# Performance work log

Measured on AMD Instinct MI355X. Metric: run time of the kernel, lower is better.

Reference implementation:

```python
import jax, jax.numpy as jnp
import numpy as np

L, H, V, T, E = 12, 12, 50257, 1024, 768
DH = E // H
EPS = 1e-5


def _ln(x, g, b):
    mu = jnp.mean(x, axis=-1, keepdims=True)
    var = jnp.mean(jnp.square(x - mu), axis=-1, keepdims=True)
    return g * (x - mu) * jax.lax.rsqrt(var + EPS) + b


def _gelu(x):
    # tanh-approx gelu as in the source
    return 0.5 * x * (1.0 + jnp.tanh(jnp.sqrt(2.0 / jnp.pi) * (x + 0.044715 * jnp.power(x, 3))))


def setup_inputs() -> dict:
    key = jax.random.key(0)
    ks = jax.random.split(key, 12)
    s = 0.02
    return {
        "x": jax.random.randint(ks[0], (8, T), 0, V),
        "tok_emb": jax.random.normal(ks[1], (V, E), jnp.float32) * s,
        "pos_emb": jax.random.normal(ks[2], (T, E), jnp.float32) * s,
        "ln1_g": jnp.ones((L, E), jnp.float32),
        "ln1_b": jnp.zeros((L, E), jnp.float32),
        "Wqkv": jax.random.normal(ks[3], (L, E, 3 * E), jnp.float32) * s,
        "bqkv": jnp.zeros((L, 3 * E), jnp.float32),
        "Wo": jax.random.normal(ks[4], (L, E, E), jnp.float32) * s,
        "bo": jnp.zeros((L, E), jnp.float32),
        "ln2_g": jnp.ones((L, E), jnp.float32),
        "ln2_b": jnp.zeros((L, E), jnp.float32),
        "W1": jax.random.normal(ks[5], (L, E, 4 * E), jnp.float32) * s,
        "b1": jnp.zeros((L, 4 * E), jnp.float32),
        "W2": jax.random.normal(ks[6], (L, 4 * E, E), jnp.float32) * s,
        "b2": jnp.zeros((L, E), jnp.float32),
        "lnf_g": jnp.ones((E,), jnp.float32),
        "lnf_b": jnp.zeros((E,), jnp.float32),
    }


def _gpt2(x, tok_emb, pos_emb, ln1_g, ln1_b, Wqkv, bqkv, Wo, bo,
          ln2_g, ln2_b, W1, b1, W2, b2, lnf_g, lnf_b):
    B, S = x.shape
    h = tok_emb[x] + pos_emb[:S][None, :, :]  # [B,S,E]
    mask = (jnp.arange(S)[:, None] >= jnp.arange(S)[None, :]).astype(jnp.float32)  # [S,S]
    mask = mask[None, None]  # [1,1,S,S]
    scale = jax.lax.rsqrt(jnp.float32(DH))
    for l in range(L):
        a = _ln(h, ln1_g[l], ln1_b[l])
        qkv = jnp.einsum('bse,ef->bsf', a, Wqkv[l]) + bqkv[l]
        q, k, v = jnp.split(qkv, 3, axis=-1)
        q = q.reshape(B, S, H, DH).transpose(0, 2, 1, 3)
        k = k.reshape(B, S, H, DH).transpose(0, 2, 1, 3)
        v = v.reshape(B, S, H, DH).transpose(0, 2, 1, 3)
        w = jnp.einsum('bhqd,bhkd->bhqk', q, k) * scale
        w = w * mask - 1e10 * (1.0 - mask)
        w = jax.nn.softmax(w, axis=-1)
        ctx = jnp.einsum('bhqk,bhkd->bhqd', w, v)
        ctx = ctx.transpose(0, 2, 1, 3).reshape(B, S, E)
        h = h + jnp.einsum('bse,ef->bsf', ctx, Wo[l]) + bo[l]
        a2 = _ln(h, ln2_g[l], ln2_b[l])
        ff = _gelu(jnp.einsum('bse,ef->bsf', a2, W1[l]) + b1[l])
        h = h + jnp.einsum('bsf,fe->bse', ff, W2[l]) + b2[l]
    h = _ln(h, lnf_g, lnf_b)
    last = h[:, -1, :]  # [B,E]
    return jnp.matmul(last, tok_emb.T)  # [B,V]


def reference(x, tok_emb, pos_emb, ln1_g, ln1_b, Wqkv, bqkv, Wo, bo,
              ln2_g, ln2_b, W1, b1, W2, b2, lnf_g, lnf_b):
    return _gpt2(x, tok_emb, pos_emb, ln1_g, ln1_b, Wqkv, bqkv, Wo, bo,
                 ln2_g, ln2_b, W1, b1, W2, b2, lnf_g, lnf_b)
```

## Files before the change

kernel.cpp:

```cpp
#include <hip/hip_runtime.h>
#include <math.h>

#define LNUM 12
#define HNUM 12
#define EMB 768
#define TSEQ 1024
#define BBATCH 8
#define VOCAB 50257
#define NTOK (BBATCH*TSEQ)

typedef unsigned short u16;
typedef __bf16 bf16_8 __attribute__((ext_vector_type(8)));
typedef float f32x4 __attribute__((ext_vector_type(4)));

__device__ __forceinline__ u16 f2bf(float f){
  unsigned u = __float_as_uint(f);
  u += 0x7fffu + ((u >> 16) & 1u);
  return (u16)(u >> 16);
}
__device__ __forceinline__ float wred(float v){
  #pragma unroll
  for (int m = 32; m; m >>= 1) v += __shfl_xor(v, m, 64);
  return v;
}

#define GLOAD_LDS16(g, l) \
  __builtin_amdgcn_global_load_lds((const __attribute__((address_space(1))) void*)(g), \
                                   (__attribute__((address_space(3))) void*)(l), 16, 0, 0)

template<int N> struct WCst { static constexpr int val = N; };

__global__ __launch_bounds__(256) void tcvt_kernel(const float* __restrict__ src,
                                                   u16* __restrict__ dst, int K, int N){
  __shared__ float tile[32][33];
  size_t off = (size_t)blockIdx.z * K * N;
  const float* s = src + off;
  u16* d = dst + off;
  int n0 = blockIdx.x * 32, k0 = blockIdx.y * 32;
  int tx = threadIdx.x & 31, ty = threadIdx.x >> 5;
  #pragma unroll
  for (int i = 0; i < 4; i++)
    tile[ty + i*8][tx] = s[(size_t)(k0 + ty + i*8) * N + n0 + tx];
  __syncthreads();
  #pragma unroll
  for (int i = 0; i < 4; i++){
    int n = ty + i*8;
    d[(size_t)(n0 + n) * K + k0 + tx] = f2bf(tile[tx][n]);
  }
}

__global__ __launch_bounds__(256) void embed_kernel(const int* __restrict__ x,
    const float* __restrict__ tok, const float* __restrict__ pos, float* __restrict__ h){
  int row = blockIdx.x;
  int t = row & (TSEQ - 1);
  int id = x[row];
  const float* te = tok + (size_t)id * EMB;
  const float* pe = pos + (size_t)t * EMB;
  float* hr = h + (size_t)row * EMB;
  for (int i = threadIdx.x; i < EMB; i += 256) hr[i] = te[i] + pe[i];
}

template<int OBF, int LAST>
__global__ __launch_bounds__(256) void ln_kernel(const float* __restrict__ x,
    const float* __restrict__ g, const float* __restrict__ b, void* __restrict__ out){
  int orow, row;
  if (LAST){ orow = blockIdx.x; row = blockIdx.x * TSEQ + (TSEQ - 1); }
  else     { orow = row = blockIdx.x; }
  const float* xr = x + (size_t)row * EMB;
  int tid = threadIdx.x;
  int wave = tid >> 6, lane = tid & 63;
  float v[3];
  float s = 0.f;
  #pragma unroll
  for (int i = 0; i < 3; i++){ v[i] = xr[tid + i*256]; s += v[i]; }
  __shared__ float red[4];
  s = wred(s);
  if (lane == 0) red[wave] = s;
  __syncthreads();
  float mu = (red[0] + red[1] + red[2] + red[3]) * (1.f / EMB);
  float ss = 0.f;
  #pragma unroll
  for (int i = 0; i < 3; i++){ float d = v[i] - mu; ss += d * d; }
  __syncthreads();
  ss = wred(ss);
  if (lane == 0) red[wave] = ss;
  __syncthreads();
  float var = (red[0] + red[1] + red[2] + red[3]) * (1.f / EMB);
  float rs = rsqrtf(var + 1e-5f);
  #pragma unroll
  for (int i = 0; i < 3; i++){
    int e = tid + i*256;
    float o = g[e] * (v[i] - mu) * rs + b[e];
    if (OBF) ((u16*)out)[(size_t)orow * EMB + e] = f2bf(o);
    else     ((float*)out)[(size_t)orow * EMB + e] = o;
  }
}

template<int EPI>
__global__ __launch_bounds__(512, 2) void gemm256(const u16* __restrict__ A,
    const u16* __restrict__ Bt, const float* __restrict__ bias,
    const float* __restrict__ resid, void* __restrict__ outp, int K, int N){
  constexpr int SLOTE = 32 * 512;
  __shared__ __align__(16) u16 lds[3 * SLOTE];
  const int tid  = threadIdx.x;
  const int wave = tid >> 6, lane = tid & 63;
  const int q15  = lane & 15, ko = lane >> 4;
  const int wm   = wave >> 2, wn = wave & 3;
  const int nwg = (int)gridDim.x, cpx = nwg >> 3, d = (int)blockIdx.x;
  const int orig = (d & 7) * cpx + (d >> 3);
  const int NBN = N >> 8;
  const int bn = orig % NBN, bm = orig / NBN;
  const int NT = K >> 5;

  const u16* gA = A  + (size_t)(bm*256 + wave*32 + q15) * K + ko * 8;
  const u16* gB = Bt + (size_t)(bn*256 + wave*32 + q15) * K + ko * 8;

#define STAGE(tt, so) do { \
    int _t = (tt); \
    GLOAD_LDS16(gA + (size_t)_t*32,                 lds + (so) + (wave*2    )*512); \
    GLOAD_LDS16(gA + (size_t)_t*32 + (size_t)16*K,  lds + (so) + (wave*2 + 1)*512); \
    GLOAD_LDS16(gB + (size_t)_t*32,                 lds + (so) + (16 + wave*2    )*512); \
    GLOAD_LDS16(gB + (size_t)_t*32 + (size_t)16*K,  lds + (so) + (16 + wave*2 + 1)*512); \
  } while (0)

  f32x4 acc[8][4];
  #pragma unroll
  for (int i = 0; i < 8; i++)
    #pragma unroll
    for (int j = 0; j < 4; j++){ f32x4 z = {0.f,0.f,0.f,0.f}; acc[i][j] = z; }

  auto tile = [&](int t, auto wc, bool dostage, bool dosync){
    if (dostage) STAGE(t + 2, ((t + 2) % 3) * SLOTE);
    const u16* sl = lds + (t % 3) * SLOTE;
    bf16_8 af[8], bfr[4];
    #pragma unroll
    for (int mi = 0; mi < 8; mi++)
      af[mi] = *(const bf16_8*)(sl + (wm*8 + mi) * 512 + lane * 8);
    #pragma unroll
    for (int ni = 0; ni < 4; ni++)
      bfr[ni] = *(const bf16_8*)(sl + (16 + wn*4 + ni) * 512 + lane * 8);
    __builtin_amdgcn_s_setprio(1);
    #pragma unroll
    for (int mi = 0; mi < 8; mi++)
      #pragma unroll
      for (int ni = 0; ni < 4; ni++)
        acc[mi][ni] = __builtin_amdgcn_mfma_f32_16x16x32_bf16(af[mi], bfr[ni], acc[mi][ni], 0, 0, 0);
    __builtin_amdgcn_s_setprio(0);
    if (dosync){
      asm volatile("s_waitcnt vmcnt(%0)" :: "n"(decltype(wc)::val) : "memory");
      __builtin_amdgcn_sched_barrier(0);
      __builtin_amdgcn_s_barrier();
      __builtin_amdgcn_sched_barrier(0);
    }
  };

  STAGE(0, 0);
  STAGE(1, SLOTE);
  asm volatile("s_waitcnt vmcnt(4)" ::: "memory");
  __builtin_amdgcn_sched_barrier(0);
  __builtin_amdgcn_s_barrier();
  __builtin_amdgcn_sched_barrier(0);

  for (int t = 0; t < NT - 2; ++t) tile(t, WCst<4>{}, true, true);
  tile(NT - 2, WCst<0>{}, false, true);
  tile(NT - 1, WCst<0>{}, false, false);
#undef STAGE

  const int colb = bn*256 + wn*64;
  const int rowb = bm*256 + wm*128;
  #pragma unroll
  for (int ni = 0; ni < 4; ni++){
    int col = colb + ni*16 + q15;
    float bv = bias[col];
    #pragma unroll
    for (int mi = 0; mi < 8; mi++){
      #pragma unroll
      for (int j = 0; j < 4; j++){
        int row = rowb + mi*16 + ko*4 + j;
        float v = acc[mi][ni][j] + bv;
        if (EPI == 1) v += resid[(size_t)row * N + col];
        if (EPI == 2){
          float y = 0.7978845608028654f * (v + 0.044715f * v * v * v);
          float e = __expf(fminf(2.f * y, 80.f));
          v = v * e / (e + 1.f);
        }
        if (EPI == 3 && col < 768) v *= 0.125f;
        if (EPI == 2 || EPI == 3) ((u16*)outp)[(size_t)row * N + col] = f2bf(v);
        else                      ((float*)outp)[(size_t)row * N + col] = v;
      }
    }
  }
}

__global__ __launch_bounds__(256) void vtrans_kernel(const u16* __restrict__ qkvb,
                                                     u16* __restrict__ vt){
  int wave = threadIdx.x >> 6, lane = threadIdx.x & 63;
  int bh = blockIdx.y, b = bh / HNUM, h = bh - b * HNUM;
  int t0 = blockIdx.x * 16 + wave * 4;
  const u16* src = qkvb + (size_t)b * TSEQ * 2304 + 1536 + h * 64 + lane;
  unsigned long long w = 0;
  #pragma unroll
  for (int i = 0; i < 4; i++)
    w |= (unsigned long long)src[(size_t)(t0 + i) * 2304] << (16 * i);
  *(unsigned long long*)(vt + ((size_t)bh * 64 + lane) * TSEQ + t0) = w;
}

__global__ __launch_bounds__(256, 2) void attn_mfma(const u16* __restrict__ qkvb,
                                                    const u16* __restrict__ vt,
                                                    u16* __restrict__ ctx){
  __shared__ u16 plds[4][64][40];
  const int wave = threadIdx.x >> 6, lane = threadIdx.x & 63;
  const int g = lane >> 4, q15 = lane & 15;
  const int bh = blockIdx.y, b = bh / HNUM, h = bh - b * HNUM;
  const int q0 = ((int)gridDim.x - 1 - (int)blockIdx.x) * 256 + wave * 64;
  const u16* qk  = qkvb + (size_t)b * TSEQ * 2304 + h * 64;
  const u16* vtb = vt + (size_t)bh * 64 * TSEQ;

#define LOADKV(kb_, kd, vd) do { \
    _Pragma("unroll") \
    for (int _kf = 0; _kf < 2; _kf++) \
      _Pragma("unroll") \
      for (int _kc = 0; _kc < 2; _kc++) \
        kd[_kf][_kc] = *(const bf16_8*)(qk + (size_t)((kb_) + _kf*16 + q15) * 2304 + 768 + _kc*32 + g*8); \
    _Pragma("unroll") \
    for (int _dc = 0; _dc < 4; _dc++) \
      vd[_dc] = *(const bf16_8*)(vtb + (size_t)(_dc*16 + q15) * TSEQ + (kb_) + g*8); \
  } while (0)

  bf16_8 qfr[4][2];
  #pragma unroll
  for (int qf = 0; qf < 4; qf++)
    #pragma unroll
    for (int kc = 0; kc < 2; kc++)
      qfr[qf][kc] = *(const bf16_8*)(qk + (size_t)(q0 + qf*16 + q15) * 2304 + kc*32 + g*8);

  f32x4 oacc[4][4];
  #pragma unroll
  for (int i = 0; i < 4; i++)
    #pragma unroll
    for (int j = 0; j < 4; j++){ f32x4 z = {0.f,0.f,0.f,0.f}; oacc[i][j] = z; }
  float mx[4] = {-1e30f,-1e30f,-1e30f,-1e30f}, lsum[4] = {0.f,0.f,0.f,0.f};

  const int kbmax = q0 + 32;
  bf16_8 kcur[2][2], vcur[4];
  LOADKV(0, kcur, vcur);

  for (int kb = 0; kb <= kbmax; kb += 32){
    bf16_8 knxt[2][2], vnxt[4];
    if (kb < kbmax) LOADKV(kb + 32, knxt, vnxt);

    f32x4 s[2][4];
    #pragma unroll
    for (int kf = 0; kf < 2; kf++)
      #pragma unroll
      for (int qf = 0; qf < 4; qf++){
        f32x4 z = {0.f,0.f,0.f,0.f};
        z = __builtin_amdgcn_mfma_f32_16x16x32_bf16(kcur[kf][0], qfr[qf][0], z, 0, 0, 0);
        z = __builtin_amdgcn_mfma_f32_16x16x32_bf16(kcur[kf][1], qfr[qf][1], z, 0, 0, 0);
        s[kf][qf] = z;
      }

    if (kb + 31 > q0){
      #pragma unroll
      for (int kf = 0; kf < 2; kf++)
        #pragma unroll
        for (int qf = 0; qf < 4; qf++)
          #pragma unroll
          for (int j = 0; j < 4; j++)
            if (kb + kf*16 + g*4 + j > q0 + qf*16 + q15) s[kf][qf][j] = -1e30f;
    }

    #pragma unroll
    for (int qf = 0; qf < 4; qf++){
      float sm = -1e30f;
      #pragma unroll
      for (int kf = 0; kf < 2; kf++)
        #pragma unroll
        for (int j = 0; j < 4; j++) sm = fmaxf(sm, s[kf][qf][j]);
      sm = fmaxf(sm, __shfl_xor(sm, 16, 64));
      sm = fmaxf(sm, __shfl_xor(sm, 32, 64));
      float mn = fmaxf(mx[qf], sm);
      float c = __expf(mx[qf] - mn);
      mx[qf] = mn;
      float ps = 0.f;
      unsigned long long pw[2];
      #pragma unroll
      for (int kf = 0; kf < 2; kf++){
        unsigned long long w = 0;
        #pragma unroll
        for (int j = 0; j < 4; j++){
          float p = __expf(s[kf][qf][j] - mn);
          ps += p;
          w |= (unsigned long long)f2bf(p) << (16 * j);
        }
        pw[kf] = w;
      }
      ps += __shfl_xor(ps, 16, 64);
      ps += __shfl_xor(ps, 32, 64);
      lsum[qf] = lsum[qf] * c + ps;
      *(unsigned long long*)&plds[wave][qf*16 + q15][g*4]      = pw[0];
      *(unsigned long long*)&plds[wave][qf*16 + q15][16 + g*4] = pw[1];
      #pragma unroll
      for (int j = 0; j < 4; j++){
        float cr = __shfl(c, g*4 + j, 64);
        #pragma unroll
        for (int dc = 0; dc < 4; dc++) oacc[qf][dc][j] *= cr;
      }
    }

    asm volatile("s_waitcnt lgkmcnt(0)" ::: "memory");
    __builtin_amdgcn_sched_barrier(0);

    bf16_8 pa[4];
    #pragma unroll
    for (int qf = 0; qf < 4; qf++)
      pa[qf] = *(const bf16_8*)&plds[wave][qf*16 + q15][g*8];
    #pragma unroll
    for (int qf = 0; qf < 4; qf++)
      #pragma unroll
      for (int dc = 0; dc < 4; dc++)
        oacc[qf][dc] = __builtin_amdgcn_mfma_f32_16x16x32_bf16(pa[qf], vcur[dc], oacc[qf][dc], 0, 0, 0);

    if (kb < kbmax){
      #pragma unroll
      for (int kf = 0; kf < 2; kf++)
        #pragma unroll
        for (int kc = 0; kc < 2; kc++) kcur[kf][kc] = knxt[kf][kc];
      #pragma unroll
      for (int dc = 0; dc < 4; dc++) vcur[dc] = vnxt[dc];
    }
  }
#undef LOADKV

  u16* cb = ctx + ((size_t)(b * TSEQ + q0)) * EMB + h * 64;
  #pragma unroll
  for (int qf = 0; qf < 4; qf++){
    float inv = 1.f / lsum[qf];
    #pragma unroll
    for (int j = 0; j < 4; j++){
      float ir = __shfl(inv, g*4 + j, 64);
      int row = qf*16 + g*4 + j;
      #pragma unroll
      for (int dc = 0; dc < 4; dc++)
        cb[(size_t)row * EMB + dc*16 + q15] = f2bf(oacc[qf][dc][j] * ir);
    }
  }
}

__global__ __launch_bounds__(256) void logits_kernel(const float* __restrict__ last,
    const float* __restrict__ tok, float* __restrict__ out){
  __shared__ float ls[BBATCH * EMB];
  for (int i = threadIdx.x; i < BBATCH * EMB; i += 256) ls[i] = last[i];
  __syncthreads();
  int wave = threadIdx.x >> 6, lane = threadIdx.x & 63;
  int v = blockIdx.x * 4 + wave;
  if (v >= VOCAB) return;
  const float* tp = tok + (size_t)v * EMB;
  float acc[BBATCH];
  #pragma unroll
  for (int b = 0; b < BBATCH; b++) acc[b] = 0.f;
  #pragma unroll
  for (int i = 0; i < EMB/64; i++){
    float tv = tp[i*64 + lane];
    #pragma unroll
    for (int b = 0; b < BBATCH; b++) acc[b] += tv * ls[b*EMB + i*64 + lane];
  }
  #pragma unroll
  for (int b = 0; b < BBATCH; b++){
    float r = wred(acc[b]);
    if (lane == 0) out[(size_t)b * VOCAB + v] = r;
  }
}

extern "C" void kernel_launch(void* const* d_in, const int* in_sizes, int n_in,
                              void* d_out, int out_size, void* d_ws, size_t ws_size,
                              hipStream_t stream){
  const int*   x    = (const int*)  d_in[0];
  const float* tok  = (const float*)d_in[1];
  const float* pos  = (const float*)d_in[2];
  const float* ln1g = (const float*)d_in[3];
  const float* ln1b = (const float*)d_in[4];
  const float* Wqkv = (const float*)d_in[5];
  const float* bqkv = (const float*)d_in[6];
  const float* Wo   = (const float*)d_in[7];
  const float* bo   = (const float*)d_in[8];
  const float* ln2g = (const float*)d_in[9];
  const float* ln2b = (const float*)d_in[10];
  const float* W1   = (const float*)d_in[11];
  const float* b1   = (const float*)d_in[12];
  const float* W2   = (const float*)d_in[13];
  const float* b2   = (const float*)d_in[14];
  const float* lnfg = (const float*)d_in[15];
  const float* lnfb = (const float*)d_in[16];

  char* p = (char*)d_ws;
  u16* wqkvT = (u16*)p;  p += (size_t)LNUM*2304*768*2;
  u16* woT   = (u16*)p;  p += (size_t)LNUM*768*768*2;
  u16* w1T   = (u16*)p;  p += (size_t)LNUM*3072*768*2;
  u16* w2T   = (u16*)p;  p += (size_t)LNUM*768*3072*2;
  float* h   = (float*)p; p += (size_t)NTOK*EMB*4;
  u16* abuf  = (u16*)p;  p += (size_t)NTOK*EMB*2;
  void* tmp  = (void*)p; p += (size_t)NTOK*2304*4;
  u16* vt    = (u16*)p;  p += (size_t)BBATCH*HNUM*64*TSEQ*2;
  float* lastb = (float*)p; p += (size_t)BBATCH*EMB*4;
  if (ws_size < (size_t)(p - (char*)d_ws)) return;

  tcvt_kernel<<<dim3(2304/32, 768/32, LNUM), 256, 0, stream>>>(Wqkv, wqkvT, 768, 2304);
  tcvt_kernel<<<dim3(768/32,  768/32, LNUM), 256, 0, stream>>>(Wo,   woT,   768, 768);
  tcvt_kernel<<<dim3(3072/32, 768/32, LNUM), 256, 0, stream>>>(W1,   w1T,   768, 3072);
  tcvt_kernel<<<dim3(768/32, 3072/32, LNUM), 256, 0, stream>>>(W2,   w2T,   3072, 768);
  embed_kernel<<<NTOK, 256, 0, stream>>>(x, tok, pos, h);

  u16* qkvb = (u16*)tmp;
  u16* ff   = (u16*)tmp;
  for (int l = 0; l < LNUM; l++){
    ln_kernel<1,0><<<NTOK, 256, 0, stream>>>(h, ln1g + l*EMB, ln1b + l*EMB, abuf);
    gemm256<3><<<(2304/256)*(NTOK/256), 512, 0, stream>>>(
        abuf, wqkvT + (size_t)l*2304*768, bqkv + (size_t)l*2304, nullptr, qkvb, 768, 2304);
    vtrans_kernel<<<dim3(TSEQ/16, BBATCH*HNUM), 256, 0, stream>>>(qkvb, vt);
    attn_mfma<<<dim3(TSEQ/256, BBATCH*HNUM), 256, 0, stream>>>(qkvb, vt, abuf);
    gemm256<1><<<(768/256)*(NTOK/256), 512, 0, stream>>>(
        abuf, woT + (size_t)l*768*768, bo + (size_t)l*768, h, h, 768, 768);
    ln_kernel<1,0><<<NTOK, 256, 0, stream>>>(h, ln2g + l*EMB, ln2b + l*EMB, abuf);
    gemm256<2><<<(3072/256)*(NTOK/256), 512, 0, stream>>>(
        abuf, w1T + (size_t)l*3072*768, b1 + (size_t)l*3072, nullptr, ff, 768, 3072);
    gemm256<1><<<(768/256)*(NTOK/256), 512, 0, stream>>>(
        ff, w2T + (size_t)l*768*3072, b2 + (size_t)l*768, h, h, 3072, 768);
  }
  ln_kernel<0,1><<<BBATCH, 256, 0, stream>>>(h, lnfg, lnfb, lastb);
  logits_kernel<<<(VOCAB + 3)/4, 256, 0, stream>>>(lastb, tok, (float*)d_out);
}
```

Measured before the change: 4.878 ms.

## Split-K residual GEMMs into partials and fuse residual add with LayerNorm

Replaces the 256x256 GEMM with a templated 128-row tile GEMM whose wave count, epilogue and split-K factor are template parameters. The N=768 projections (Wo, W2) now run split-K by 2 and write two fp32 partial buffers, which raises the block count for these narrow GEMMs. A new ln_merge kernel sums the residual, both partials and the bias, writes h, and applies the next LayerNorm in the same pass, removing the separate LN launches and the residual read in the GEMM epilogue. The cost is extra fp32 partial traffic, a new workspace layout with aliased buffers, and a smaller tile that gives less reuse per block.

```diff
diff --git a/kernel.cpp b/kernel.cpp
--- a/kernel.cpp
+++ b/kernel.cpp
@@ -60,17 +60,12 @@
   for (int i = threadIdx.x; i < EMB; i += 256) hr[i] = te[i] + pe[i];
 }
 
-template<int OBF, int LAST>
 __global__ __launch_bounds__(256) void ln_kernel(const float* __restrict__ x,
-    const float* __restrict__ g, const float* __restrict__ b, void* __restrict__ out){
-  int orow, row;
-  if (LAST){ orow = blockIdx.x; row = blockIdx.x * TSEQ + (TSEQ - 1); }
-  else     { orow = row = blockIdx.x; }
+    const float* __restrict__ g, const float* __restrict__ b, u16* __restrict__ out){
+  int row = blockIdx.x;
   const float* xr = x + (size_t)row * EMB;
-  int tid = threadIdx.x;
-  int wave = tid >> 6, lane = tid & 63;
-  float v[3];
-  float s = 0.f;
+  int tid = threadIdx.x, wave = tid >> 6, lane = tid & 63;
+  float v[3]; float s = 0.f;
   #pragma unroll
   for (int i = 0; i < 3; i++){ v[i] = xr[tid + i*256]; s += v[i]; }
   __shared__ float red[4];
@@ -90,37 +85,85 @@
   #pragma unroll
   for (int i = 0; i < 3; i++){
     int e = tid + i*256;
+    out[(size_t)row * EMB + e] = f2bf(g[e] * (v[i] - mu) * rs + b[e]);
+  }
+}
+
+template<int LASTF>
+__global__ __launch_bounds__(256) void ln_merge(const float* __restrict__ x,
+    const float* __restrict__ p0, const float* __restrict__ p1,
+    const float* __restrict__ pbias, const float* __restrict__ g,
+    const float* __restrict__ b, float* __restrict__ hout, void* __restrict__ lnout){
+  int orow = blockIdx.x;
+  int row = LASTF ? (orow * TSEQ + (TSEQ - 1)) : orow;
+  int tid = threadIdx.x, wave = tid >> 6, lane = tid & 63;
+  float v[3]; float s = 0.f;
+  #pragma unroll
+  for (int i = 0; i < 3; i++){
+    int e = tid + i*256;
+    size_t idx = (size_t)row * EMB + e;
+    v[i] = x[idx] + p0[idx] + p1[idx] + pbias[e];
+    if (!LASTF) hout[idx] = v[i];
+    s += v[i];
+  }
+  __shared__ float red[4];
+  s = wred(s);
+  if (lane == 0) red[wave] = s;
+  __syncthreads();
+  float mu = (red[0] + red[1] + red[2] + red[3]) * (1.f / EMB);
+  float ss = 0.f;
+  #pragma unroll
+  for (int i = 0; i < 3; i++){ float d = v[i] - mu; ss += d * d; }
+  __syncthreads();
+  ss = wred(ss);
+  if (lane == 0) red[wave] = ss;
+  __syncthreads();
+  float var = (red[0] + red[1] + red[2] + red[3]) * (1.f / EMB);
+  float rs = rsqrtf(var + 1e-5f);
+  #pragma unroll
+  for (int i = 0; i < 3; i++){
+    int e = tid + i*256;
     float o = g[e] * (v[i] - mu) * rs + b[e];
-    if (OBF) ((u16*)out)[(size_t)orow * EMB + e] = f2bf(o);
-    else     ((float*)out)[(size_t)orow * EMB + e] = o;
-  }
-}
-
-template<int EPI>
-__global__ __launch_bounds__(512, 2) void gemm256(const u16* __restrict__ A,
+    if (LASTF) ((float*)lnout)[(size_t)orow * EMB + e] = o;
+    else       ((u16*)lnout)[(size_t)orow * EMB + e] = f2bf(o);
+  }
+}
+
+template<int NW, int EPI, int KS>
+__global__ __launch_bounds__(NW*64, 2) void gemm_wt(const u16* __restrict__ A,
     const u16* __restrict__ Bt, const float* __restrict__ bias,
-    const float* __restrict__ resid, void* __restrict__ outp, int K, int N){
-  constexpr int SLOTE = 32 * 512;
+    void* __restrict__ out0, void* __restrict__ out1, int K, int N){
+  constexpr int BN    = NW * 64;
+  constexpr int BGR   = BN / 16;
+  constexpr int NA    = 8 / NW;
+  constexpr int LOADS = NA + 4;
+  constexpr int SLOTE = (8 + BGR) * 512;
   __shared__ __align__(16) u16 lds[3 * SLOTE];
   const int tid  = threadIdx.x;
   const int wave = tid >> 6, lane = tid & 63;
   const int q15  = lane & 15, ko = lane >> 4;
-  const int wm   = wave >> 2, wn = wave & 3;
-  const int nwg = (int)gridDim.x, cpx = nwg >> 3, d = (int)blockIdx.x;
-  const int orig = (d & 7) * cpx + (d >> 3);
-  const int NBN = N >> 8;
-  const int bn = orig % NBN, bm = orig / NBN;
-  const int NT = K >> 5;
-
-  const u16* gA = A  + (size_t)(bm*256 + wave*32 + q15) * K + ko * 8;
-  const u16* gB = Bt + (size_t)(bn*256 + wave*32 + q15) * K + ko * 8;
-
-#define STAGE(tt, so) do { \
+  const int nwg = (int)gridDim.x, cpx = nwg >> 3, dd = (int)blockIdx.x;
+  const int orig = (dd & 7) * cpx + (dd >> 3);
+  const int NBN = N / BN;
+  const int bn = orig % NBN;
+  const int rest = orig / NBN;
+  const int ks = (KS > 1) ? (rest % KS) : 0;
+  const int bm = (KS > 1) ? (rest / KS) : rest;
+  const int K2 = K / KS;
+  const int NT = K2 >> 5;
+
+  const u16* gA0 = A  + (size_t)(bm*128 + wave*NA*16 + q15) * K + (size_t)ks*K2 + ko*8;
+  const u16* gB0 = Bt + (size_t)(bn*BN  + wave*4*16  + q15) * K + (size_t)ks*K2 + ko*8;
+
+#define STAGE(tt) do { \
     int _t = (tt); \
-    GLOAD_LDS16(gA + (size_t)_t*32,                 lds + (so) + (wave*2    )*512); \
-    GLOAD_LDS16(gA + (size_t)_t*32 + (size_t)16*K,  lds + (so) + (wave*2 + 1)*512); \
-    GLOAD_LDS16(gB + (size_t)_t*32,                 lds + (so) + (16 + wave*2    )*512); \
-    GLOAD_LDS16(gB + (size_t)_t*32 + (size_t)16*K,  lds + (so) + (16 + wave*2 + 1)*512); \
+    u16* _sl = lds + (_t % 3) * SLOTE; \
+    _Pragma("unroll") \
+    for (int _i = 0; _i < NA; _i++) \
+      GLOAD_LDS16(gA0 + (size_t)_i*16*K + _t*32, _sl + (wave*NA + _i) * 512); \
+    _Pragma("unroll") \
+    for (int _i = 0; _i < 4; _i++) \
+      GLOAD_LDS16(gB0 + (size_t)_i*16*K + _t*32, _sl + (8 + wave*4 + _i) * 512); \
   } while (0)
 
   f32x4 acc[8][4];
@@ -130,21 +173,23 @@
     for (int j = 0; j < 4; j++){ f32x4 z = {0.f,0.f,0.f,0.f}; acc[i][j] = z; }
 
   auto tile = [&](int t, auto wc, bool dostage, bool dosync){
-    if (dostage) STAGE(t + 2, ((t + 2) % 3) * SLOTE);
     const u16* sl = lds + (t % 3) * SLOTE;
-    bf16_8 af[8], bfr[4];
+    bf16_8 af[8], bf[4];
     #pragma unroll
     for (int mi = 0; mi < 8; mi++)
-      af[mi] = *(const bf16_8*)(sl + (wm*8 + mi) * 512 + lane * 8);
+      af[mi] = *(const bf16_8*)(sl + mi * 512 + lane * 8);
     #pragma unroll
     for (int ni = 0; ni < 4; ni++)
-      bfr[ni] = *(const bf16_8*)(sl + (16 + wn*4 + ni) * 512 + lane * 8);
+      bf[ni] = *(const bf16_8*)(sl + (8 + wave*4 + ni) * 512 + lane * 8);
+    if (dostage) STAGE(t + 2);
+    asm volatile("s_waitcnt lgkmcnt(0)" ::: "memory");
+    __builtin_amdgcn_sched_barrier(0);
     __builtin_amdgcn_s_setprio(1);
     #pragma unroll
     for (int mi = 0; mi < 8; mi++)
       #pragma unroll
       for (int ni = 0; ni < 4; ni++)
-        acc[mi][ni] = __builtin_amdgcn_mfma_f32_16x16x32_bf16(af[mi], bfr[ni], acc[mi][ni], 0, 0, 0);
+        acc[mi][ni] = __builtin_amdgcn_mfma_f32_16x16x32_bf16(af[mi], bf[ni], acc[mi][ni], 0, 0, 0);
     __builtin_amdgcn_s_setprio(0);
     if (dosync){
       asm volatile("s_waitcnt vmcnt(%0)" :: "n"(decltype(wc)::val) : "memory");
@@ -154,39 +199,42 @@
     }
   };
 
-  STAGE(0, 0);
-  STAGE(1, SLOTE);
-  asm volatile("s_waitcnt vmcnt(4)" ::: "memory");
+  STAGE(0);
+  STAGE(1);
+  asm volatile("s_waitcnt vmcnt(%0)" :: "n"(LOADS) : "memory");
   __builtin_amdgcn_sched_barrier(0);
   __builtin_amdgcn_s_barrier();
   __builtin_amdgcn_sched_barrier(0);
 
-  for (int t = 0; t < NT - 2; ++t) tile(t, WCst<4>{}, true, true);
+  for (int t = 0; t < NT - 2; ++t) tile(t, WCst<LOADS>{}, true, true);
   tile(NT - 2, WCst<0>{}, false, true);
   tile(NT - 1, WCst<0>{}, false, false);
 #undef STAGE
 
-  const int colb = bn*256 + wn*64;
-  const int rowb = bm*256 + wm*128;
+  const int colb = bn*BN + wave*64;
+  const int rowb = bm*128;
   #pragma unroll
   for (int ni = 0; ni < 4; ni++){
     int col = colb + ni*16 + q15;
-    float bv = bias[col];
+    float bv = (EPI == 0) ? 0.f : bias[col];
     #pragma unroll
     for (int mi = 0; mi < 8; mi++){
       #pragma unroll
       for (int j = 0; j < 4; j++){
         int row = rowb + mi*16 + ko*4 + j;
         float v = acc[mi][ni][j] + bv;
-        if (EPI == 1) v += resid[(size_t)row * N + col];
-        if (EPI == 2){
+        if (EPI == 0){
+          float* o = ks ? (float*)out1 : (float*)out0;
+          o[(size_t)row * N + col] = v;
+        } else if (EPI == 2){
           float y = 0.7978845608028654f * (v + 0.044715f * v * v * v);
           float e = __expf(fminf(2.f * y, 80.f));
           v = v * e / (e + 1.f);
+          ((u16*)out0)[(size_t)row * N + col] = f2bf(v);
+        } else {
+          if (col < 768) v *= 0.125f;
+          ((u16*)out0)[(size_t)row * N + col] = f2bf(v);
         }
-        if (EPI == 3 && col < 768) v *= 0.125f;
-        if (EPI == 2 || EPI == 3) ((u16*)outp)[(size_t)row * N + col] = f2bf(v);
-        else                      ((float*)outp)[(size_t)row * N + col] = v;
       }
     }
   }
@@ -400,10 +448,20 @@
   u16* w2T   = (u16*)p;  p += (size_t)LNUM*768*3072*2;
   float* h   = (float*)p; p += (size_t)NTOK*EMB*4;
   u16* abuf  = (u16*)p;  p += (size_t)NTOK*EMB*2;
-  void* tmp  = (void*)p; p += (size_t)NTOK*2304*4;
-  u16* vt    = (u16*)p;  p += (size_t)BBATCH*HNUM*64*TSEQ*2;
+  u16* vt    = (u16*)p;  p += (size_t)NTOK*EMB*2;
+  char* tmp  = p;        p += (size_t)NTOK*2304*4;
   float* lastb = (float*)p; p += (size_t)BBATCH*EMB*4;
   if (ws_size < (size_t)(p - (char*)d_ws)) return;
+
+  const size_t SZ_A  = (size_t)NTOK*EMB*2;
+  u16*   aln  = (u16*)tmp;
+  u16*   qkvb = (u16*)(tmp + SZ_A);
+  float* pp0  = (float*)(tmp + SZ_A);
+  float* pp1  = (float*)(tmp + SZ_A + (size_t)NTOK*EMB*4);
+  u16*   a2   = (u16*)(tmp + SZ_A + 2*(size_t)NTOK*EMB*4);
+  u16*   ff   = (u16*)tmp;
+  float* pf0  = (float*)(tmp + 4*SZ_A);
+  float* pf1  = (float*)abuf;
 
   tcvt_kernel<<<dim3(2304/32, 768/32, LNUM), 256, 0, stream>>>(Wqkv, wqkvT, 768, 2304);
   tcvt_kernel<<<dim3(768/32,  768/32, LNUM), 256, 0, stream>>>(Wo,   woT,   768, 768);
@@ -411,22 +469,25 @@
   tcvt_kernel<<<dim3(768/32, 3072/32, LNUM), 256, 0, stream>>>(W2,   w2T,   3072, 768);
   embed_kernel<<<NTOK, 256, 0, stream>>>(x, tok, pos, h);
 
-  u16* qkvb = (u16*)tmp;
-  u16* ff   = (u16*)tmp;
+  ln_kernel<<<NTOK, 256, 0, stream>>>(h, ln1g, ln1b, aln);
   for (int l = 0; l < LNUM; l++){
-    ln_kernel<1,0><<<NTOK, 256, 0, stream>>>(h, ln1g + l*EMB, ln1b + l*EMB, abuf);
-    gemm256<3><<<(2304/256)*(NTOK/256), 512, 0, stream>>>(
-        abuf, wqkvT + (size_t)l*2304*768, bqkv + (size_t)l*2304, nullptr, qkvb, 768, 2304);
+    gemm_wt<4,3,1><<<(NTOK/128)*(2304/256), 256, 0, stream>>>(
+        aln, wqkvT + (size_t)l*2304*768, bqkv + (size_t)l*2304, qkvb, nullptr, 768, 2304);
     vtrans_kernel<<<dim3(TSEQ/16, BBATCH*HNUM), 256, 0, stream>>>(qkvb, vt);
     attn_mfma<<<dim3(TSEQ/256, BBATCH*HNUM), 256, 0, stream>>>(qkvb, vt, abuf);
-    gemm256<1><<<(768/256)*(NTOK/256), 512, 0, stream>>>(
-        abuf, woT + (size_t)l*768*768, bo + (size_t)l*768, h, h, 768, 768);
-    ln_kernel<1,0><<<NTOK, 256, 0, stream>>>(h, ln2g + l*EMB, ln2b + l*EMB, abuf);
-    gemm256<2><<<(3072/256)*(NTOK/256), 512, 0, stream>>>(
-        abuf, w1T + (size_t)l*3072*768, b1 + (size_t)l*3072, nullptr, ff, 768, 3072);
-    gemm256<1><<<(768/256)*(NTOK/256), 512, 0, stream>>>(
-        ff, w2T + (size_t)l*768*3072, b2 + (size_t)l*768, h, h, 3072, 768);
-  }
-  ln_kernel<0,1><<<BBATCH, 256, 0, stream>>>(h, lnfg, lnfb, lastb);
+    gemm_wt<2,0,2><<<(NTOK/128)*(768/128)*2, 128, 0, stream>>>(
+        abuf, woT + (size_t)l*768*768, nullptr, pp0, pp1, 768, 768);
+    ln_merge<0><<<NTOK, 256, 0, stream>>>(h, pp0, pp1, bo + (size_t)l*768,
+        ln2g + (size_t)l*EMB, ln2b + (size_t)l*EMB, h, a2);
+    gemm_wt<4,2,1><<<(NTOK/128)*(3072/256), 256, 0, stream>>>(
+        a2, w1T + (size_t)l*3072*768, b1 + (size_t)l*3072, ff, nullptr, 768, 3072);
+    gemm_wt<2,0,2><<<(NTOK/128)*(768/128)*2, 128, 0, stream>>>(
+        ff, w2T + (size_t)l*768*3072, nullptr, pf0, pf1, 3072, 768);
+    if (l < LNUM - 1)
+      ln_merge<0><<<NTOK, 256, 0, stream>>>(h, pf0, pf1, b2 + (size_t)l*768,
+          ln1g + (size_t)(l+1)*EMB, ln1b + (size_t)(l+1)*EMB, h, aln);
+  }
+  ln_merge<1><<<BBATCH, 256, 0, stream>>>(h, pf0, pf1, b2 + (size_t)(LNUM-1)*768,
+      lnfg, lnfb, nullptr, lastb);
   logits_kernel<<<(VOCAB + 3)/4, 256, 0, stream>>>(lastb, tok, (float*)d_out);
 }
```

After: 4.355 ms. 10.7% less time.
